# Kernel tuning notes

Hardware: AMD Instinct MI355X
Metric: run time of the kernel (lower is better)

Reference implementation:

```python
import jax, jax.numpy as jnp
import numpy as np

N_NODES = 50000
N_EDGES = 800000
IN_DIM = 64
HID_DIM = 128
OUT_DIM = 64
BN_EPS = 1e-5


def _glorot(key, shape):
    fan_in, fan_out = shape[0], shape[1]
    lim = (6.0 / (fan_in + fan_out)) ** 0.5
    return jax.random.uniform(key, shape, jnp.float32, -lim, lim)


def setup_inputs() -> dict:
    key = jax.random.key(0)
    ks = jax.random.split(key, 8)
    x = jax.random.normal(ks[0], (N_NODES, IN_DIM), jnp.float32)
    edge_index = jax.random.randint(ks[1], (2, N_EDGES), 0, N_NODES, jnp.int32)
    return {
        "x": x,
        "edge_index": edge_index,
        # SAGEConv1: lin_l (applied to aggregated neighbors, has bias), lin_r (root, no bias)
        "W1l": _glorot(ks[2], (IN_DIM, HID_DIM)),
        "b1": jnp.zeros((HID_DIM,), jnp.float32),
        "W1r": _glorot(ks[3], (IN_DIM, HID_DIM)),
        # BatchNorm1d params
        "gamma": jnp.ones((HID_DIM,), jnp.float32),
        "beta": jnp.zeros((HID_DIM,), jnp.float32),
        # SAGEConv2
        "W2l": _glorot(ks[4], (HID_DIM, OUT_DIM)),
        "b2": jnp.zeros((OUT_DIM,), jnp.float32),
        "W2r": _glorot(ks[5], (HID_DIM, OUT_DIM)),
    }


def _sage_conv(h, src, dst, Wl, b, Wr, deg_inv):
    # mean-aggregate neighbor features per destination node
    agg = jax.ops.segment_sum(h[src], dst, num_segments=N_NODES)  # [N, d]
    agg = agg * deg_inv[:, None]
    return agg @ Wl + b + h @ Wr


def reference(x, edge_index, W1l, b1, W1r, gamma, beta, W2l, b2, W2r):
    src, dst = edge_index[0], edge_index[1]
    deg = jax.ops.segment_sum(jnp.ones((N_EDGES,), jnp.float32), dst,
                              num_segments=N_NODES)
    deg_inv = jnp.where(deg > 0, 1.0 / jnp.maximum(deg, 1.0), 0.0)

    h = _sage_conv(x, src, dst, W1l, b1, W1r, deg_inv)  # [N, hid]
    # BatchNorm1d (training mode: batch stats over nodes, biased variance)
    mu = jnp.mean(h, axis=0)
    var = jnp.mean((h - mu) ** 2, axis=0)
    h = (h - mu) * jax.lax.rsqrt(var + BN_EPS) * gamma + beta
    h = jax.nn.relu(h)
    out = _sage_conv(h, src, dst, W2l, b2, W2r, deg_inv)  # [N, out]
    return out
```

## Files before the change

kernel.cpp:

```cpp
#include <hip/hip_runtime.h>

#define NN 50000
#define NE 800000
#define HID 128
#define OUTD 64
#define NBK 200
#define BWID 250
#define CAP 5120
#define TILE_E 4096
#define XB 3125
#define HB 196

typedef __attribute__((ext_vector_type(8))) short bf16x8;
typedef __attribute__((ext_vector_type(4))) float f32x4;

static __device__ __forceinline__ unsigned short f2bf(float f) {
    unsigned u = __float_as_uint(f);
    unsigned r = (u + 0x7FFFu + ((u >> 16) & 1u)) >> 16;
    return (unsigned short)r;
}
static __device__ __forceinline__ float bflo(unsigned u) { return __uint_as_float(u << 16); }
static __device__ __forceinline__ float bfhi(unsigned u) { return __uint_as_float(u & 0xffff0000u); }

__global__ __launch_bounds__(256) void prep_kernel(
    const float* __restrict__ x, unsigned short* __restrict__ A1,
    const float* __restrict__ W1l, const float* __restrict__ W1r,
    const float* __restrict__ W2l, const float* __restrict__ W2r,
    unsigned short* __restrict__ BT1, unsigned short* __restrict__ BT2,
    int* __restrict__ gcur, float* __restrict__ sums)
{
    int blk = blockIdx.x, tid = threadIdx.x;
    if (blk < XB) {
        int idx = blk * 256 + tid;
        int n = idx >> 4, q = idx & 15;
        float4 v = ((const float4*)x)[idx];
        ushort4 o;
        o.x = f2bf(v.x); o.y = f2bf(v.y); o.z = f2bf(v.z); o.w = f2bf(v.w);
        *(ushort4*)(A1 + (size_t)n * 128 + 64 + q * 4) = o;
    } else if (blk < XB + 64) {
        int idx = (blk - XB) * 256 + tid;
        int j = idx >> 7, k = idx & 127;
        float v1 = (k < 64) ? W1l[k * HID + j] : W1r[(k - 64) * HID + j];
        BT1[j * 128 + k] = f2bf(v1);
        float v2 = (j < 64) ? W2l[k * OUTD + j] : W2r[k * OUTD + (j - 64)];
        BT2[j * 128 + k] = f2bf(v2);
    } else {
        if (tid < NBK) gcur[tid] = tid * CAP;
        sums[tid] = 0.f;
        sums[tid + 256] = 0.f;
    }
}

__global__ __launch_bounds__(256) void binA_kernel(const int* __restrict__ src,
                                                   const int* __restrict__ dst,
                                                   int* __restrict__ gcur,
                                                   int2* __restrict__ pairs) {
    __shared__ int lcnt[NBK];
    __shared__ int lbase[NBK];
    int tid = threadIdx.x;
    int e0 = blockIdx.x * TILE_E;
    for (int i = tid; i < NBK; i += 256) lcnt[i] = 0;
    __syncthreads();
    int s[16], d[16], loc[16];
#pragma unroll
    for (int i = 0; i < 16; i++) {
        int e = e0 + i * 256 + tid;
        if (e < NE) {
            s[i] = __builtin_nontemporal_load(&src[e]);
            d[i] = __builtin_nontemporal_load(&dst[e]);
            loc[i] = atomicAdd(&lcnt[d[i] / BWID], 1);
        }
    }
    __syncthreads();
    for (int b = tid; b < NBK; b += 256)
        lbase[b] = atomicAdd(&gcur[b], lcnt[b]);
    __syncthreads();
#pragma unroll
    for (int i = 0; i < 16; i++) {
        int e = e0 + i * 256 + tid;
        if (e < NE)
            pairs[lbase[d[i] / BWID] + loc[i]] = make_int2(s[i], d[i]);
    }
}

__global__ __launch_bounds__(256) void binB_kernel(const int2* __restrict__ pairs,
                                                   const int* __restrict__ gcur,
                                                   int* __restrict__ startp,
                                                   int* __restrict__ endp,
                                                   int* __restrict__ perm) {
    __shared__ int lcnt[BWID];
    __shared__ int tmp[256];
    __shared__ int lcur[BWID];
    int b = blockIdx.x, tid = threadIdx.x;
    int lo = b * CAP;
    int hi = gcur[b];
    int base = b * BWID;
    for (int i = tid; i < BWID; i += 256) lcnt[i] = 0;
    __syncthreads();
    for (int i = lo + tid; i < hi; i += 256)
        atomicAdd(&lcnt[pairs[i].y - base], 1);
    __syncthreads();
    int v = (tid < BWID) ? lcnt[tid] : 0;
    tmp[tid] = v;
    __syncthreads();
    for (int off = 1; off < 256; off <<= 1) {
        int t = (tid >= off) ? tmp[tid - off] : 0;
        __syncthreads();
        tmp[tid] += t;
        __syncthreads();
    }
    if (tid < BWID) {
        int s = lo + tmp[tid] - v;
        lcur[tid] = s;
        startp[base + tid] = s;
        endp[base + tid] = s + v;
    }
    __syncthreads();
    for (int i = lo + tid; i < hi; i += 256) {
        int2 p = pairs[i];
        int pos = atomicAdd(&lcur[p.y - base], 1);
        perm[pos] = p.x;
    }
}

template<int MODE>
__global__ __launch_bounds__(256) void agg_gather_b(
    const unsigned short* __restrict__ feat, int fstride, int foff,
    const int* __restrict__ startp, const int* __restrict__ endp,
    const int* __restrict__ perm,
    unsigned short* __restrict__ outb, int ostride, int ooff,
    float* __restrict__ outf)
{
    int wave = (blockIdx.x * blockDim.x + threadIdx.x) >> 6;
    if (wave >= NN) return;
    int lane = threadIdx.x & 63;
    int g = lane >> 3;
    int q = lane & 7;
    int rs = startp[wave];
    int re = endp[wave];
    float acc[8];
#pragma unroll
    for (int t = 0; t < 8; t++) acc[t] = 0.f;
    int i = rs + g;
    for (; i + 8 < re; i += 16) {
        int s0 = perm[i];
        int s1 = perm[i + 8];
        uint4 v0 = *(const uint4*)(feat + (size_t)s0 * fstride + foff + q * 8);
        uint4 v1 = *(const uint4*)(feat + (size_t)s1 * fstride + foff + q * 8);
        acc[0] += bflo(v0.x); acc[1] += bfhi(v0.x);
        acc[2] += bflo(v0.y); acc[3] += bfhi(v0.y);
        acc[4] += bflo(v0.z); acc[5] += bfhi(v0.z);
        acc[6] += bflo(v0.w); acc[7] += bfhi(v0.w);
        acc[0] += bflo(v1.x); acc[1] += bfhi(v1.x);
        acc[2] += bflo(v1.y); acc[3] += bfhi(v1.y);
        acc[4] += bflo(v1.z); acc[5] += bfhi(v1.z);
        acc[6] += bflo(v1.w); acc[7] += bfhi(v1.w);
    }
    if (i < re) {
        int s0 = perm[i];
        uint4 v0 = *(const uint4*)(feat + (size_t)s0 * fstride + foff + q * 8);
        acc[0] += bflo(v0.x); acc[1] += bfhi(v0.x);
        acc[2] += bflo(v0.y); acc[3] += bfhi(v0.y);
        acc[4] += bflo(v0.z); acc[5] += bfhi(v0.z);
        acc[6] += bflo(v0.w); acc[7] += bfhi(v0.w);
    }
#pragma unroll
    for (int t = 0; t < 8; t++) {
        acc[t] += __shfl_xor(acc[t], 8, 64);
        acc[t] += __shfl_xor(acc[t], 16, 64);
        acc[t] += __shfl_xor(acc[t], 32, 64);
    }
    if (g == 0) {
        int cnt = re - rs;
        float inv = (cnt > 0) ? (1.0f / (float)cnt) : 0.f;
        if (MODE == 0) {
            uint4 o;
            o.x = (unsigned)f2bf(acc[0] * inv) | ((unsigned)f2bf(acc[1] * inv) << 16);
            o.y = (unsigned)f2bf(acc[2] * inv) | ((unsigned)f2bf(acc[3] * inv) << 16);
            o.z = (unsigned)f2bf(acc[4] * inv) | ((unsigned)f2bf(acc[5] * inv) << 16);
            o.w = (unsigned)f2bf(acc[6] * inv) | ((unsigned)f2bf(acc[7] * inv) << 16);
            *(uint4*)(outb + (size_t)wave * ostride + ooff + q * 8) = o;
        } else {
            float4* op = (float4*)(outf + (size_t)wave * 64 + q * 8);
            float4 o0 = op[0], o1 = op[1];
            o0.x += acc[0] * inv; o0.y += acc[1] * inv;
            o0.z += acc[2] * inv; o0.w += acc[3] * inv;
            o1.x += acc[4] * inv; o1.y += acc[5] * inv;
            o1.z += acc[6] * inv; o1.w += acc[7] * inv;
            op[0] = o0; op[1] = o1;
        }
    }
}

template<bool IS1>
__global__ __launch_bounds__(256) void conv_mfma_kernel(
    const unsigned short* __restrict__ A, const unsigned short* __restrict__ BT,
    const float* __restrict__ bias,
    unsigned short* __restrict__ outb, float* __restrict__ outf,
    float* __restrict__ sums, float* __restrict__ sumsq)
{
    __shared__ float red_s[4][128];
    __shared__ float red_q[4][128];
    int tid = threadIdx.x;
    int wid = tid >> 6, lane = tid & 63;
    int m = lane & 15, ko = lane >> 4;
    int gw = blockIdx.x * 4 + wid;
    int jh = gw & 1;
    int tstride = (gridDim.x * 4) >> 1;
    const int tiles = NN / 16;
    bf16x8 b[4][4];
    const unsigned short* bbase = BT + (size_t)(jh * 64 + m) * 128 + ko * 8;
#pragma unroll
    for (int jg = 0; jg < 4; jg++)
#pragma unroll
        for (int ks = 0; ks < 4; ks++)
            b[jg][ks] = *(const bf16x8*)(bbase + jg * 16 * 128 + ks * 32);
    float bj[4];
#pragma unroll
    for (int jg = 0; jg < 4; jg++)
        bj[jg] = IS1 ? bias[jh * 64 + jg * 16 + m] : (jh ? bias[jg * 16 + m] : 0.f);
    float s_sum[4] = {0.f, 0.f, 0.f, 0.f}, s_sq[4] = {0.f, 0.f, 0.f, 0.f};
    int tile = gw >> 1;
    bf16x8 a[4];
    if (tile < tiles) {
        const unsigned short* arow = A + (size_t)(tile * 16 + m) * 128 + ko * 8;
#pragma unroll
        for (int ks = 0; ks < 4; ks++) a[ks] = *(const bf16x8*)(arow + ks * 32);
    }
    while (tile < tiles) {
        int nxt = tile + tstride;
        bf16x8 an[4];
        if (nxt < tiles) {
            const unsigned short* arow = A + (size_t)(nxt * 16 + m) * 128 + ko * 8;
#pragma unroll
            for (int ks = 0; ks < 4; ks++) an[ks] = *(const bf16x8*)(arow + ks * 32);
        }
        int n0 = tile * 16;
#pragma unroll
        for (int jg = 0; jg < 4; jg++) {
            f32x4 acc = {0.f, 0.f, 0.f, 0.f};
#pragma unroll
            for (int ks = 0; ks < 4; ks++)
                acc = __builtin_amdgcn_mfma_f32_16x16x32_bf16(a[ks], b[jg][ks], acc, 0, 0, 0);
            int j = jh * 64 + jg * 16 + m;
#pragma unroll
            for (int r = 0; r < 4; r++) {
                int n = n0 + ko * 4 + r;
                float v = acc[r];
                if (IS1) {
                    v += bj[jg];
                    outb[(size_t)n * 128 + j] = f2bf(v);
                    s_sum[jg] += v;
                    s_sq[jg] += v * v;
                } else {
                    if (jh == 0) outb[(size_t)n * 64 + j] = f2bf(v);
                    else         outf[(size_t)n * 64 + (j - 64)] = v + bj[jg];
                }
            }
        }
#pragma unroll
        for (int ks = 0; ks < 4; ks++) a[ks] = an[ks];
        tile = nxt;
    }
    if (IS1) {
        for (int i = tid; i < 512; i += 256) {
            ((float*)red_s)[i] = 0.f;
            ((float*)red_q)[i] = 0.f;
        }
        __syncthreads();
#pragma unroll
        for (int jg = 0; jg < 4; jg++) {
            float v = s_sum[jg];
            v += __shfl_xor(v, 16, 64);
            v += __shfl_xor(v, 32, 64);
            float w = s_sq[jg];
            w += __shfl_xor(w, 16, 64);
            w += __shfl_xor(w, 32, 64);
            if (lane < 16) {
                red_s[wid][jh * 64 + jg * 16 + lane] = v;
                red_q[wid][jh * 64 + jg * 16 + lane] = w;
            }
        }
        __syncthreads();
        if (tid < 128) {
            float v = red_s[0][tid] + red_s[1][tid] + red_s[2][tid] + red_s[3][tid];
            atomicAdd(&sums[tid], v);
        } else {
            int j = tid - 128;
            float v = red_q[0][j] + red_q[1][j] + red_q[2][j] + red_q[3][j];
            atomicAdd(&sumsq[j], v);
        }
    }
}

__global__ void bnstat_kernel(const float* __restrict__ sums, const float* __restrict__ sumsq,
                              const float* __restrict__ gamma, const float* __restrict__ beta,
                              float* __restrict__ scale, float* __restrict__ shift) {
    int c = threadIdx.x;
    if (c < HID) {
        float inv_n = 1.0f / (float)NN;
        float mu = sums[c] * inv_n;
        float var = sumsq[c] * inv_n - mu * mu;
        float s = gamma[c] * rsqrtf(var + 1e-5f);
        scale[c] = s;
        shift[c] = beta[c] - mu * s;
    }
}

__global__ void bnapply_kernel(const unsigned short* __restrict__ hpreb,
                               const float* __restrict__ scale, const float* __restrict__ shift,
                               unsigned short* __restrict__ A1) {
    int idx = blockIdx.x * 256 + threadIdx.x;
    if (idx >= NN * 16) return;
    int q = idx & 15;
    int j0 = q * 8;
    uint4 v = ((const uint4*)hpreb)[idx];
    float f[8];
    f[0] = bflo(v.x); f[1] = bfhi(v.x);
    f[2] = bflo(v.y); f[3] = bfhi(v.y);
    f[4] = bflo(v.z); f[5] = bfhi(v.z);
    f[6] = bflo(v.w); f[7] = bfhi(v.w);
#pragma unroll
    for (int t = 0; t < 8; t++) {
        float h = f[t] * scale[j0 + t] + shift[j0 + t];
        f[t] = h > 0.f ? h : 0.f;
    }
    uint4 o;
    o.x = (unsigned)f2bf(f[0]) | ((unsigned)f2bf(f[1]) << 16);
    o.y = (unsigned)f2bf(f[2]) | ((unsigned)f2bf(f[3]) << 16);
    o.z = (unsigned)f2bf(f[4]) | ((unsigned)f2bf(f[5]) << 16);
    o.w = (unsigned)f2bf(f[6]) | ((unsigned)f2bf(f[7]) << 16);
    ((uint4*)A1)[idx] = o;
}

extern "C" void kernel_launch(void* const* d_in, const int* in_sizes, int n_in,
                              void* d_out, int out_size, void* d_ws, size_t ws_size,
                              hipStream_t stream) {
    const float* x     = (const float*)d_in[0];
    const int*   ei    = (const int*)d_in[1];
    const float* W1l   = (const float*)d_in[2];
    const float* b1    = (const float*)d_in[3];
    const float* W1r   = (const float*)d_in[4];
    const float* gamma = (const float*)d_in[5];
    const float* beta  = (const float*)d_in[6];
    const float* W2l   = (const float*)d_in[7];
    const float* b2    = (const float*)d_in[8];
    const float* W2r   = (const float*)d_in[9];
    float* out = (float*)d_out;

    char* wsb = (char*)d_ws;
    int*   gcur   = (int*)wsb;
    float* sums   = (float*)(gcur + 256);
    float* sumsq  = sums + 128;
    float* scale  = sums + 256;
    float* shift  = sums + 384;
    int*   startp = (int*)(sums + 512);
    int*   endp   = startp + NN;
    int*   perm   = endp + NN;
    unsigned short* A1    = (unsigned short*)(perm + NBK * CAP);
    unsigned short* hpreb = A1 + (size_t)NN * 128;
    unsigned short* BT1   = hpreb + (size_t)NN * 128;
    unsigned short* BT2   = BT1 + 128 * 128;
    int2*  pairs  = (int2*)hpreb;

    const int* srcp = ei;
    const int* dstp = ei + NE;

    const int GB = (NN * 64 + 255) / 256;
    const int CB = 512;

    prep_kernel<<<XB + 64 + 1, 256, 0, stream>>>(x, A1, W1l, W1r, W2l, W2r,
                                                 BT1, BT2, gcur, sums);
    binA_kernel<<<HB, 256, 0, stream>>>(srcp, dstp, gcur, pairs);
    binB_kernel<<<NBK, 256, 0, stream>>>(pairs, gcur, startp, endp, perm);

    agg_gather_b<0><<<GB, 256, 0, stream>>>(A1, 128, 64, startp, endp, perm,
                                            A1, 128, 0, nullptr);
    conv_mfma_kernel<true><<<CB, 256, 0, stream>>>(A1, BT1, b1, hpreb, nullptr, sums, sumsq);
    bnstat_kernel<<<1, 128, 0, stream>>>(sums, sumsq, gamma, beta, scale, shift);
    bnapply_kernel<<<XB, 256, 0, stream>>>(hpreb, scale, shift, A1);
    conv_mfma_kernel<false><<<CB, 256, 0, stream>>>(A1, BT2, b2, hpreb, out, nullptr, nullptr);
    agg_gather_b<1><<<GB, 256, 0, stream>>>(hpreb, 64, 0, startp, endp, perm,
                                            nullptr, 0, 0, out);
}
```

Before: 201.8 us.

## Transpose MFMA output for vectorized stores and fold BN stats into apply

The MFMA operands are swapped so each lane holds four consecutive output columns of one node. That allows packed 8-byte bf16 stores and 16-byte float4 stores instead of scattered 2-byte and 4-byte writes. The per-column stat reduction now shuffles across the 16 node lanes, and each lane keeps 16 partial sums and 16 sums of squares. The single-block bnstat kernel is removed: every bnapply block recomputes scale and shift into shared memory, saving one launch at the cost of some redundant reads of the sums.

```diff
diff --git a/kernel.cpp b/kernel.cpp
--- a/kernel.cpp
+++ b/kernel.cpp
@@ -47,7 +47,6 @@
     } else {
         if (tid < NBK) gcur[tid] = tid * CAP;
         sums[tid] = 0.f;
-        sums[tid + 256] = 0.f;
     }
 }
 
@@ -203,27 +202,32 @@
     __shared__ float red_q[4][128];
     int tid = threadIdx.x;
     int wid = tid >> 6, lane = tid & 63;
-    int m = lane & 15, ko = lane >> 4;
+    int nl = lane & 15, ko = lane >> 4;
     int gw = blockIdx.x * 4 + wid;
     int jh = gw & 1;
     int tstride = (gridDim.x * 4) >> 1;
     const int tiles = NN / 16;
     bf16x8 b[4][4];
-    const unsigned short* bbase = BT + (size_t)(jh * 64 + m) * 128 + ko * 8;
+    const unsigned short* bbase = BT + (size_t)(jh * 64 + nl) * 128 + ko * 8;
 #pragma unroll
     for (int jg = 0; jg < 4; jg++)
 #pragma unroll
         for (int ks = 0; ks < 4; ks++)
             b[jg][ks] = *(const bf16x8*)(bbase + jg * 16 * 128 + ks * 32);
-    float bj[4];
-#pragma unroll
-    for (int jg = 0; jg < 4; jg++)
-        bj[jg] = IS1 ? bias[jh * 64 + jg * 16 + m] : (jh ? bias[jg * 16 + m] : 0.f);
-    float s_sum[4] = {0.f, 0.f, 0.f, 0.f}, s_sq[4] = {0.f, 0.f, 0.f, 0.f};
+    float4 bias4[4];
+#pragma unroll
+    for (int jg = 0; jg < 4; jg++) {
+        if (IS1)        bias4[jg] = *(const float4*)(bias + jh * 64 + jg * 16 + ko * 4);
+        else if (jh)    bias4[jg] = *(const float4*)(bias + jg * 16 + ko * 4);
+        else            bias4[jg] = make_float4(0.f, 0.f, 0.f, 0.f);
+    }
+    float s_sum[16], s_sq[16];
+#pragma unroll
+    for (int t = 0; t < 16; t++) { s_sum[t] = 0.f; s_sq[t] = 0.f; }
     int tile = gw >> 1;
     bf16x8 a[4];
     if (tile < tiles) {
-        const unsigned short* arow = A + (size_t)(tile * 16 + m) * 128 + ko * 8;
+        const unsigned short* arow = A + (size_t)(tile * 16 + nl) * 128 + ko * 8;
 #pragma unroll
         for (int ks = 0; ks < 4; ks++) a[ks] = *(const bf16x8*)(arow + ks * 32);
     }
@@ -231,30 +235,39 @@
         int nxt = tile + tstride;
         bf16x8 an[4];
         if (nxt < tiles) {
-            const unsigned short* arow = A + (size_t)(nxt * 16 + m) * 128 + ko * 8;
+            const unsigned short* arow = A + (size_t)(nxt * 16 + nl) * 128 + ko * 8;
 #pragma unroll
             for (int ks = 0; ks < 4; ks++) an[ks] = *(const bf16x8*)(arow + ks * 32);
         }
-        int n0 = tile * 16;
+        int n_g = tile * 16 + nl;
 #pragma unroll
         for (int jg = 0; jg < 4; jg++) {
             f32x4 acc = {0.f, 0.f, 0.f, 0.f};
 #pragma unroll
             for (int ks = 0; ks < 4; ks++)
-                acc = __builtin_amdgcn_mfma_f32_16x16x32_bf16(a[ks], b[jg][ks], acc, 0, 0, 0);
-            int j = jh * 64 + jg * 16 + m;
-#pragma unroll
-            for (int r = 0; r < 4; r++) {
-                int n = n0 + ko * 4 + r;
-                float v = acc[r];
-                if (IS1) {
-                    v += bj[jg];
-                    outb[(size_t)n * 128 + j] = f2bf(v);
-                    s_sum[jg] += v;
-                    s_sq[jg] += v * v;
+                acc = __builtin_amdgcn_mfma_f32_16x16x32_bf16(b[jg][ks], a[ks], acc, 0, 0, 0);
+            float v0 = acc[0] + bias4[jg].x;
+            float v1 = acc[1] + bias4[jg].y;
+            float v2 = acc[2] + bias4[jg].z;
+            float v3 = acc[3] + bias4[jg].w;
+            if (IS1) {
+                s_sum[jg * 4 + 0] += v0; s_sq[jg * 4 + 0] += v0 * v0;
+                s_sum[jg * 4 + 1] += v1; s_sq[jg * 4 + 1] += v1 * v1;
+                s_sum[jg * 4 + 2] += v2; s_sq[jg * 4 + 2] += v2 * v2;
+                s_sum[jg * 4 + 3] += v3; s_sq[jg * 4 + 3] += v3 * v3;
+                uint2 pk;
+                pk.x = (unsigned)f2bf(v0) | ((unsigned)f2bf(v1) << 16);
+                pk.y = (unsigned)f2bf(v2) | ((unsigned)f2bf(v3) << 16);
+                *(uint2*)(outb + (size_t)n_g * 128 + jh * 64 + jg * 16 + ko * 4) = pk;
+            } else {
+                if (jh == 0) {
+                    uint2 pk;
+                    pk.x = (unsigned)f2bf(v0) | ((unsigned)f2bf(v1) << 16);
+                    pk.y = (unsigned)f2bf(v2) | ((unsigned)f2bf(v3) << 16);
+                    *(uint2*)(outb + (size_t)n_g * 64 + jg * 16 + ko * 4) = pk;
                 } else {
-                    if (jh == 0) outb[(size_t)n * 64 + j] = f2bf(v);
-                    else         outf[(size_t)n * 64 + (j - 64)] = v + bj[jg];
+                    float4 o = make_float4(v0, v1, v2, v3);
+                    *(float4*)(outf + (size_t)n_g * 64 + jg * 16 + ko * 4) = o;
                 }
             }
         }
@@ -270,15 +283,22 @@
         __syncthreads();
 #pragma unroll
         for (int jg = 0; jg < 4; jg++) {
-            float v = s_sum[jg];
-            v += __shfl_xor(v, 16, 64);
-            v += __shfl_xor(v, 32, 64);
-            float w = s_sq[jg];
-            w += __shfl_xor(w, 16, 64);
-            w += __shfl_xor(w, 32, 64);
-            if (lane < 16) {
-                red_s[wid][jh * 64 + jg * 16 + lane] = v;
-                red_q[wid][jh * 64 + jg * 16 + lane] = w;
+#pragma unroll
+            for (int r = 0; r < 4; r++) {
+                float v = s_sum[jg * 4 + r];
+                v += __shfl_xor(v, 1, 64);
+                v += __shfl_xor(v, 2, 64);
+                v += __shfl_xor(v, 4, 64);
+                v += __shfl_xor(v, 8, 64);
+                float w = s_sq[jg * 4 + r];
+                w += __shfl_xor(w, 1, 64);
+                w += __shfl_xor(w, 2, 64);
+                w += __shfl_xor(w, 4, 64);
+                w += __shfl_xor(w, 8, 64);
+                if (nl == 0) {
+                    red_s[wid][jh * 64 + jg * 16 + ko * 4 + r] = v;
+                    red_q[wid][jh * 64 + jg * 16 + ko * 4 + r] = w;
+                }
             }
         }
         __syncthreads();
@@ -293,24 +313,24 @@
     }
 }
 
-__global__ void bnstat_kernel(const float* __restrict__ sums, const float* __restrict__ sumsq,
-                              const float* __restrict__ gamma, const float* __restrict__ beta,
-                              float* __restrict__ scale, float* __restrict__ shift) {
-    int c = threadIdx.x;
-    if (c < HID) {
+__global__ __launch_bounds__(256) void bnapply_kernel(
+    const unsigned short* __restrict__ hpreb,
+    const float* __restrict__ sums, const float* __restrict__ sumsq,
+    const float* __restrict__ gamma, const float* __restrict__ beta,
+    unsigned short* __restrict__ A1)
+{
+    __shared__ float sc[128], sh[128];
+    int tid = threadIdx.x;
+    if (tid < 128) {
         float inv_n = 1.0f / (float)NN;
-        float mu = sums[c] * inv_n;
-        float var = sumsq[c] * inv_n - mu * mu;
-        float s = gamma[c] * rsqrtf(var + 1e-5f);
-        scale[c] = s;
-        shift[c] = beta[c] - mu * s;
-    }
-}
-
-__global__ void bnapply_kernel(const unsigned short* __restrict__ hpreb,
-                               const float* __restrict__ scale, const float* __restrict__ shift,
-                               unsigned short* __restrict__ A1) {
-    int idx = blockIdx.x * 256 + threadIdx.x;
+        float mu = sums[tid] * inv_n;
+        float var = sumsq[tid] * inv_n - mu * mu;
+        float s = gamma[tid] * rsqrtf(var + 1e-5f);
+        sc[tid] = s;
+        sh[tid] = beta[tid] - mu * s;
+    }
+    __syncthreads();
+    int idx = blockIdx.x * 256 + tid;
     if (idx >= NN * 16) return;
     int q = idx & 15;
     int j0 = q * 8;
@@ -322,7 +342,7 @@
     f[6] = bflo(v.w); f[7] = bfhi(v.w);
 #pragma unroll
     for (int t = 0; t < 8; t++) {
-        float h = f[t] * scale[j0 + t] + shift[j0 + t];
+        float h = f[t] * sc[j0 + t] + sh[j0 + t];
         f[t] = h > 0.f ? h : 0.f;
     }
     uint4 o;
@@ -352,9 +372,7 @@
     int*   gcur   = (int*)wsb;
     float* sums   = (float*)(gcur + 256);
     float* sumsq  = sums + 128;
-    float* scale  = sums + 256;
-    float* shift  = sums + 384;
-    int*   startp = (int*)(sums + 512);
+    int*   startp = (int*)(sums + 256);
     int*   endp   = startp + NN;
     int*   perm   = endp + NN;
     unsigned short* A1    = (unsigned short*)(perm + NBK * CAP);
@@ -377,8 +395,7 @@
     agg_gather_b<0><<<GB, 256, 0, stream>>>(A1, 128, 64, startp, endp, perm,
                                             A1, 128, 0, nullptr);
     conv_mfma_kernel<true><<<CB, 256, 0, stream>>>(A1, BT1, b1, hpreb, nullptr, sums, sumsq);
-    bnstat_kernel<<<1, 128, 0, stream>>>(sums, sumsq, gamma, beta, scale, shift);
-    bnapply_kernel<<<XB, 256, 0, stream>>>(hpreb, scale, shift, A1);
+    bnapply_kernel<<<XB, 256, 0, stream>>>(hpreb, sums, sumsq, gamma, beta, A1);
     conv_mfma_kernel<false><<<CB, 256, 0, stream>>>(A1, BT2, b2, hpreb, out, nullptr, nullptr);
     agg_gather_b<1><<<GB, 256, 0, stream>>>(hpreb, 64, 0, startp, endp, perm,
                                             nullptr, 0, 0, out);
```

After: 201.2 us. About the same (-0.3%).
